# Kernel tuning notes

Measured on AMD Instinct MI355X. Metric: run time of the kernel, lower is better.

The kernel has to match this reference:

```python
import jax, jax.numpy as jnp
import numpy as np

B, C, H, W = 64, 128, 11, 11
OUT = 16
N_SIM = 5
EPS = 1e-2


def _conv3d(x, w, b):
    # x: [b,ci,D,h,w], w: [co,ci,7,3,3], 'same' padding, ReLU
    y = jax.lax.conv_general_dilated(x, w, (1, 1, 1), [(3, 3), (1, 1), (1, 1)],
                                     dimension_numbers=('NCDHW', 'OIDHW', 'NCDHW'))
    return jax.nn.relu(y + b[None, :, None, None, None])


def _conv2d(x, w, b, dil=1):
    p = dil  # 3x3 kernel, 'same' with dilation
    y = jax.lax.conv_general_dilated(x, w, (1, 1), [(p, p), (p, p)], rhs_dilation=(dil, dil),
                                     dimension_numbers=('NCHW', 'OIHW', 'NCHW'))
    return y + b[None, :, None, None]


def _center(f):  # [b,c,h,w] -> [b,c] (center pixel)
    return f[:, :, f.shape[2] // 2, f.shape[3] // 2]


def _ratio(v):  # compute_ratio_withstep: [b,c] -> [b,1,c,c] band-ratio image
    d = v[:, None, :]
    d = jnp.where(jnp.abs(d) < EPS, EPS, d)
    return (v[:, :, None] / d)[:, None, :, :]


def _cpr(sa3d, w):  # CVT3D_2D_SA: spectral-attention collapse [b,16,D,h,w] -> [b,16,h,w]
    a = jax.nn.softmax(w, axis=-1)
    return jax.nn.relu(jnp.einsum('bodhw,od->bohw', sa3d, a))


def _sideout(f2d, w, b):  # sideout2d: mlp on center pixel features
    return _center(f2d) @ w.T + b


def _similar_sum(x, feat, n=N_SIM):
    # topk(n, largest=False) over |feat - center|, gather those pixels from x, sum them
    b, c = x.shape[0], x.shape[1]
    cv = _center(feat).reshape(b, 1, 1, 1)
    diff = jnp.abs(feat - cv).reshape(b, -1)          # [b, h*w]
    _, idx = jax.lax.top_k(-diff, n)                   # n smallest -> [b, n]
    img = x.reshape(b, c, -1)                          # [b, c, h*w]
    idx_b = jnp.broadcast_to(idx[:, None, :], (b, c, n))
    sim = jnp.take_along_axis(img, idx_b, axis=2)      # [b, c, n]
    return sim.sum(axis=2)                             # masked sum over n similar pixels


def _forward(x, w3d1, b3d1, w3d23, b3d23, cpr_w, w2d45, b2d45, seg_w, seg_b,
             so_w, so_b, sp_wa, sp_ba, sp_wb, sp_bb, sp_sw, sp_sb, fuse_para):
    sp_ct = _ratio(_center(x))                         # [b,1,c,c]
    sa1 = _conv3d(x[:, None], w3d1, b3d1)              # [b,16,C,11,11]
    sa1_2d = _cpr(sa1, cpr_w[0])
    sa2 = _conv3d(sa1, w3d23[0], b3d23[0])
    sa2_2d = _cpr(sa2, cpr_w[1])
    sa3 = _conv3d(sa2, w3d23[1], b3d23[1])
    sa3_2d = _cpr(sa3, cpr_w[2])
    sa4_2d = jax.nn.relu(_conv2d(sa3_2d, w2d45[0], b2d45[0]))
    sa5_2d = jax.nn.relu(_conv2d(sa4_2d, w2d45[1], b2d45[1]))

    feats = [sa1_2d, sa2_2d, sa3_2d, sa4_2d, sa5_2d]
    sa_sides, sp_sides = [], []
    for i, f in enumerate(feats):  # fixed 5 structurally-distinct stages
        sa_sides.append(_sideout(f, so_w[i], so_b[i]))
        act = _conv2d(f, seg_w[i], seg_b[i])           # Seg_Conv: [b,1,11,11]
        s = _similar_sum(x, act)                       # [b,C]
        img = jnp.concatenate([_ratio(s), sp_ct], 1)   # [b,2,C,C]
        y = jax.nn.relu(_conv2d(img, sp_wa[i], sp_ba[i], dil=1))
        y = jax.nn.relu(_conv2d(y, sp_wb[i], sp_bb[i], dil=2))
        sp_sides.append(_sideout(y, sp_sw[i], sp_sb[i]))

    sides = sa_sides + sp_sides
    total = sides[0] * fuse_para[0]
    for i in range(1, 10):
        total = total + fuse_para[i] * sides[i]
    return total                                       # [b, OUT]


def setup_inputs() -> dict:
    key = jax.random.key(0)
    ks = jax.random.split(key, 20)
    s = 0.05
    return {
        'x': jax.random.normal(ks[0], (B, C, H, W), jnp.float32),
        'w3d1': jax.random.normal(ks[1], (16, 1, 7, 3, 3), jnp.float32) * s,
        'b3d1': jnp.zeros((16,), jnp.float32),
        'w3d23': jax.random.normal(ks[2], (2, 16, 16, 7, 3, 3), jnp.float32) * s,
        'b3d23': jnp.zeros((2, 16), jnp.float32),
        'cpr_w': jax.random.normal(ks[3], (3, 16, C), jnp.float32) * s,
        'w2d45': jax.random.normal(ks[4], (2, 16, 16, 3, 3), jnp.float32) * s,
        'b2d45': jnp.zeros((2, 16), jnp.float32),
        'seg_w': jax.random.normal(ks[5], (5, 1, 16, 3, 3), jnp.float32) * s,
        'seg_b': jnp.zeros((5, 1), jnp.float32),
        'so_w': jax.random.normal(ks[6], (5, OUT, 16), jnp.float32) * s,
        'so_b': jnp.zeros((5, OUT), jnp.float32),
        'sp_wa': jax.random.normal(ks[7], (5, 16, 2, 3, 3), jnp.float32) * s,
        'sp_ba': jnp.zeros((5, 16), jnp.float32),
        'sp_wb': jax.random.normal(ks[8], (5, 16, 16, 3, 3), jnp.float32) * s,
        'sp_bb': jnp.zeros((5, 16), jnp.float32),
        'sp_sw': jax.random.normal(ks[9], (5, OUT, 16), jnp.float32) * s,
        'sp_sb': jnp.zeros((5, OUT), jnp.float32),
        'fuse_para': jnp.ones((15,), jnp.float32),
    }


def reference(x, w3d1, b3d1, w3d23, b3d23, cpr_w, w2d45, b2d45, seg_w, seg_b,
              so_w, so_b, sp_wa, sp_ba, sp_wb, sp_bb, sp_sw, sp_sb, fuse_para):
    return _forward(x, w3d1, b3d1, w3d23, b3d23, cpr_w, w2d45, b2d45, seg_w, seg_b,
                    so_w, so_b, sp_wa, sp_ba, sp_wb, sp_bb, sp_sw, sp_sb, fuse_para)
```

## Files before the change

### kernel.cpp

```cpp
#include <hip/hip_runtime.h>
#include <hip/hip_bf16.h>


#define F_SLICE (64 * 16 * 121)
#define PKE (64 * 121 * 134 * 16)
#define LHALF 18304
#define AREP_CV 36864

typedef _Float16 half8 __attribute__((ext_vector_type(8)));
typedef float float4v __attribute__((ext_vector_type(4)));
typedef unsigned short u16x8 __attribute__((ext_vector_type(8)));
typedef unsigned short u16x4 __attribute__((ext_vector_type(4)));

typedef __attribute__((address_space(1))) unsigned int gu32;
typedef __attribute__((address_space(3))) unsigned int lu32;

union HU { _Float16 h; unsigned short u; };

__global__ __launch_bounds__(256) void prep_kernel(
    const float* __restrict__ x, const float* __restrict__ cpr_w,
    const float* __restrict__ w3d1, const float* __restrict__ w2d45,
    const float* __restrict__ w3d23, float* __restrict__ x_t,
    float* __restrict__ a_sm, float* __restrict__ wrep1,
    float* __restrict__ wrep2d, unsigned short* __restrict__ arep) {
  const int bx = blockIdx.x, t = threadIdx.x;
  if (bx < 64) {
    __shared__ float tile[128][123];
    const int b = bx;
    const float* xb = x + (size_t)b * 128 * 121;
    for (int idx = t; idx < 128 * 121; idx += 256) {
      int c = idx / 121, p = idx - c * 121;
      tile[c][p] = xb[idx];
    }
    __syncthreads();
    float* ob = x_t + (size_t)b * 121 * 128;
    for (int idx = t; idx < 121 * 128; idx += 256) {
      int p = idx >> 7, c = idx & 127;
      ob[idx] = tile[c][p];
    }
  } else if (bx < 112) {
    __shared__ float red[128];
    const int row = bx - 64;
    float v = (t < 128) ? cpr_w[row * 128 + t] : -3.0e38f;
    if (t < 128) red[t] = v;
    __syncthreads();
    for (int s = 64; s; s >>= 1) {
      if (t < s) red[t] = fmaxf(red[t], red[t + s]);
      __syncthreads();
    }
    float m = red[0];
    __syncthreads();
    float e = (t < 128) ? expf(v - m) : 0.f;
    if (t < 128) red[t] = e;
    __syncthreads();
    for (int s = 64; s; s >>= 1) {
      if (t < s) red[t] += red[t + s];
      __syncthreads();
    }
    if (t < 128) a_sm[row * 128 + t] = e / red[0];
  } else if (bx < 134) {
    int r = (bx - 112) * 256 + t;
    if (r < 1008) {
      int j = r;
      int kw = j % 3; j /= 3;
      int o = j % 8; j /= 8;
      int kh = j % 3; j /= 3;
      int kd = j % 7; j /= 7;
      int gg = j;
      wrep1[r] = w3d1[(gg * 8 + o) * 63 + kd * 9 + kh * 3 + kw];
    } else if (r < 1008 + 4608) {
      int r2 = r - 1008;
      int o = r2 & 15;
      int uv = (r2 >> 4) % 9;
      int ic = (r2 / 144) % 16;
      int layer = r2 / 2304;
      wrep2d[r2] = w2d45[((layer * 16 + o) * 16 + ic) * 9 + uv];
    }
  } else {
    int idx = (bx - 134) * 256 + t;
    if (idx < 2 * AREP_CV) {
      int j = idx & 7;
      int lane = (idx >> 3) & 63;
      int part = (idx >> 9) & 1;
      int rem = idx >> 10;
      int chunk = rem % 36;
      int cv = rem / 36;
      int kw = chunk % 3;
      int grp = chunk / 3;
      int kdp = grp & 3;
      int kh = grp >> 2;
      int m = lane & 15, q = lane >> 4;
      int kd = 2 * kdp + (q >> 1);
      int ic = (q & 1) * 8 + j;
      float w = 0.f;
      if (kd < 7)
        w = w3d23[((cv * 16 + m) * 16 + ic) * 63 + kd * 9 + kh * 3 + kw] *
            256.f;
      _Float16 hi = (_Float16)w;
      HU out;
      out.h = (part == 0) ? hi : (_Float16)(w - (float)hi);
      arep[idx] = out.u;
    }
  }
}

__global__ __launch_bounds__(256, 4) void conv1_kernel(
    const float* __restrict__ in, const float* __restrict__ wrep,
    const float* __restrict__ bias, const float* __restrict__ al,
    unsigned short* __restrict__ pk_hi, unsigned short* __restrict__ pk_lo,
    float* __restrict__ f_out) {
  __shared__ float in_lds[18][134];
  __shared__ float red[2][16][4];
  const int t = threadIdx.x;
  const int bx = blockIdx.x;
  const int b = blockIdx.y;
  const int h = bx / 3;
  const int w0 = (bx % 3) * 4;
  const int lane = t & 63;
  const int wv = t >> 6;
  const int dh = wv & 1;
  const int dd = lane + (dh << 6);
  const int g = __builtin_amdgcn_readfirstlane(wv >> 1);
  const int oc_base = g << 3;

  float acc[8][4];
#pragma unroll
  for (int o = 0; o < 8; ++o)
#pragma unroll
    for (int c = 0; c < 4; ++c) acc[o][c] = 0.f;

  const int ds = t & 127;
  const int half = t >> 7;

  for (int r = half; r < 18; r += 2) {
    int hr = r / 6;
    int wc = r - hr * 6;
    int hh = h - 1 + hr;
    int ww = w0 - 1 + wc;
    bool ok = (hh >= 0) & (hh < 11) & (ww >= 0) & (ww < 11);
    const float* src = in + (((size_t)b) * 121 + hh * 11 + ww) * 128;
    float v = 0.f;
    if (ok && ds >= 3) v = src[ds - 3];
    in_lds[r][ds] = v;
    if (ds < 6) {
      float v2 = 0.f;
      if (ok && ds < 3) v2 = src[125 + ds];
      in_lds[r][128 + ds] = v2;
    }
  }
  __syncthreads();
  const float* wbase = wrep + g * 504;
#pragma unroll
  for (int kd = 0; kd < 7; ++kd) {
#pragma unroll
    for (int kh = 0; kh < 3; ++kh) {
      float ws[24];
      const float* wp = wbase + kd * 72 + kh * 24;
#pragma unroll
      for (int j = 0; j < 24; ++j) ws[j] = wp[j];
      float v[6];
#pragma unroll
      for (int qq = 0; qq < 6; ++qq) v[qq] = in_lds[kh * 6 + qq][dd + kd];
#pragma unroll
      for (int o = 0; o < 8; ++o)
#pragma unroll
        for (int kw = 0; kw < 3; ++kw) {
          float wv_ = ws[o * 3 + kw];
#pragma unroll
          for (int c = 0; c < 4; ++c)
            acc[o][c] = fmaf(wv_, v[kw + c], acc[o][c]);
        }
    }
  }

  const int p0 = h * 11 + w0;
#pragma unroll
  for (int o = 0; o < 8; ++o) {
    float bv = bias[oc_base + o];
#pragma unroll
    for (int c = 0; c < 4; ++c) acc[o][c] = fmaxf(acc[o][c] + bv, 0.f);
  }
#pragma unroll
  for (int c = 0; c < 4; ++c) {
    if (w0 + c < 11) {
      u16x8 hi8, lo8;
#pragma unroll
      for (int o = 0; o < 8; ++o) {
        float s = acc[o][c] * 256.f;
        _Float16 hh = (_Float16)s;
        HU a, bb;
        a.h = hh;
        bb.h = (_Float16)(s - (float)hh);
        hi8[o] = a.u;
        lo8[o] = bb.u;
      }
      size_t base = (((size_t)b * 121 + p0 + c) * 134 + dd + 3) * 16 + oc_base;
      *(u16x8*)&pk_hi[base] = hi8;
      *(u16x8*)&pk_lo[base] = lo8;
    }
  }
  if (dd < 3) {
    u16x8 z = {0, 0, 0, 0, 0, 0, 0, 0};
#pragma unroll
    for (int c = 0; c < 4; ++c) {
      if (w0 + c < 11) {
        size_t b0 = (((size_t)b * 121 + p0 + c) * 134 + dd) * 16 + oc_base;
        size_t b1 =
            (((size_t)b * 121 + p0 + c) * 134 + 131 + dd) * 16 + oc_base;
        *(u16x8*)&pk_hi[b0] = z;
        *(u16x8*)&pk_lo[b0] = z;
        *(u16x8*)&pk_hi[b1] = z;
        *(u16x8*)&pk_lo[b1] = z;
      }
    }
  }
  float alv[8];
#pragma unroll
  for (int o = 0; o < 8; ++o) alv[o] = al[(oc_base + o) * 128 + dd];
#pragma unroll
  for (int o = 0; o < 8; ++o) {
#pragma unroll
    for (int c = 0; c < 4; ++c) {
      float pv = acc[o][c] * alv[o];
#pragma unroll
      for (int off = 32; off; off >>= 1) pv += __shfl_down(pv, off, 64);
      if (lane == 0) red[dh][oc_base + o][c] = pv;
    }
  }
  __syncthreads();
  if (t < 64) {
    int oc = t >> 2, c = t & 3;
    if (w0 + c < 11)
      f_out[((size_t)b * 16 + oc) * 121 + p0 + c] =
          fmaxf(red[0][oc][c] + red[1][oc][c], 0.f);
  }
}

template <bool WRITE_PK>
__global__ __launch_bounds__(512, 2) void conv_mfma_kernel(
    const unsigned short* __restrict__ pin_hi,
    const unsigned short* __restrict__ pin_lo,
    const unsigned short* __restrict__ arep, const float* __restrict__ bias,
    const float* __restrict__ al, unsigned short* __restrict__ pout_hi,
    unsigned short* __restrict__ pout_lo, float* __restrict__ fpart) {
  __shared__ _Float16 lds[2 * LHALF];
  const int t = threadIdx.x;
  const int bx = blockIdx.x, d16 = blockIdx.y, b = blockIdx.z;
  const int lane = t & 63, wave = t >> 6;
  const int n = lane & 15, q = lane >> 4;
  const int hs = wave >> 2, wg = wave & 3;
  const int h = 2 * bx + hs;

#pragma unroll
  for (int i = 0; i < 9; ++i) {
    int u = t + i * 512;
    int lbo = __builtin_amdgcn_readfirstlane((wave << 6) + i * 512);
    if (u < 4576) {
      int part = (u >= 2288) ? 1 : 0;
      int qq = u - part * 2288;
      int pc = qq / 22;
      int dloc = qq - pc * 22;
      int panel = pc >> 1, icq = pc & 1;
      int rr = panel / 13, cc = panel - rr * 13;
      int hh = 2 * bx + rr - 1, ww = cc - 1;
      bool ok = (hh >= 0) & (hh < 11) & (ww >= 0) & (ww < 11);
      if (ok) {
        const unsigned short* srcp = part ? pin_lo : pin_hi;
        const unsigned short* g =
            &srcp[(((size_t)b * 121 + hh * 11 + ww) * 134 + d16 * 16 + dloc) *
                      16 +
                  icq * 8];
        __builtin_amdgcn_global_load_lds((const gu32*)g,
                                         (lu32*)&lds[(size_t)lbo * 8], 16, 0,
                                         0);
      } else {
        u16x8 z = {0, 0, 0, 0, 0, 0, 0, 0};
        *(u16x8*)&lds[(size_t)u * 8] = z;
      }
    }
  }
  float bias_r[4], alr[4];
#pragma unroll
  for (int r = 0; r < 4; ++r) {
    bias_r[r] = bias[q * 4 + r];
    alr[r] = al[(q * 4 + r) * 128 + d16 * 16 + n];
  }
  __syncthreads();

  const int wl0 = wg * 3;
  int cb[5], cbk[5];
  const int base_qn = (q & 1) * 176 + n * 8 + hs * 4576;
  const int kdh = (lane & 32) ? 8 : 0;
#pragma unroll
  for (int j = 0; j < 5; ++j) {
    int colj = wl0 + j;
    if (colj > 12) colj = 12;
    cb[j] = base_qn + colj * 352;
    cbk[j] = cb[j] + kdh;
  }

  float4v acc[3];
#pragma unroll
  for (int tt = 0; tt < 3; ++tt) acc[tt] = (float4v){0.f, 0.f, 0.f, 0.f};

#pragma unroll
  for (int kh = 0; kh < 3; ++kh) {
#pragma unroll
    for (int kdp = 0; kdp < 4; ++kdp) {
      half8 whi[5], wlo[5];
#pragma unroll
      for (int j = 0; j < 5; ++j) {
        int a = ((kdp < 3) ? cbk[j] : cb[j]) + kh * 4576 + kdp * 16;
        whi[j] = *(const half8*)&lds[a];
        wlo[j] = *(const half8*)&lds[a + LHALF];
      }
#pragma unroll
      for (int kw = 0; kw < 3; ++kw) {
        const int c2 = (kh * 4 + kdp) * 3 + kw;
        half8 ahi = *(const half8*)&arep[((c2 * 2 + 0) * 64 + lane) * 8];
        half8 alo = *(const half8*)&arep[((c2 * 2 + 1) * 64 + lane) * 8];
#pragma unroll
        for (int tt = 0; tt < 3; ++tt) {
          const int jj = tt + kw;
          acc[tt] = __builtin_amdgcn_mfma_f32_16x16x32_f16(ahi, whi[jj],
                                                           acc[tt], 0, 0, 0);
          acc[tt] = __builtin_amdgcn_mfma_f32_16x16x32_f16(ahi, wlo[jj],
                                                           acc[tt], 0, 0, 0);
          acc[tt] = __builtin_amdgcn_mfma_f32_16x16x32_f16(alo, whi[jj],
                                                           acc[tt], 0, 0, 0);
        }
      }
    }
  }

#pragma unroll
  for (int tt = 0; tt < 3; ++tt) {
    const int wl = wg * 3 + tt;
    if (h < 11 && wl < 11) {
      const int p = h * 11 + wl;
      float fr[4];
      u16x4 hi4, lo4;
#pragma unroll
      for (int r = 0; r < 4; ++r) {
        float sv = fmaxf(acc[tt][r] * (1.f / 65536.f) + bias_r[r], 0.f);
        fr[r] = sv * alr[r];
        if (WRITE_PK) {
          float s = sv * 256.f;
          _Float16 hh = (_Float16)s;
          HU a, bb;
          a.h = hh;
          bb.h = (_Float16)(s - (float)hh);
          hi4[r] = a.u;
          lo4[r] = bb.u;
        }
      }
      if (WRITE_PK) {
        size_t base =
            (((size_t)b * 121 + p) * 134 + d16 * 16 + n + 3) * 16 + q * 4;
        *(u16x4*)&pout_hi[base] = hi4;
        *(u16x4*)&pout_lo[base] = lo4;
        u16x4 z = {0, 0, 0, 0};
        if (d16 == 0 && n < 3) {
          size_t hb = (((size_t)b * 121 + p) * 134 + n) * 16 + q * 4;
          *(u16x4*)&pout_hi[hb] = z;
          *(u16x4*)&pout_lo[hb] = z;
        }
        if (d16 == 7 && n >= 13) {
          size_t hb = (((size_t)b * 121 + p) * 134 + n + 118) * 16 + q * 4;
          *(u16x4*)&pout_hi[hb] = z;
          *(u16x4*)&pout_lo[hb] = z;
        }
      }
#pragma unroll
      for (int r = 0; r < 4; ++r) {
        float v = fr[r];
        v += __shfl_xor(v, 1, 64);
        v += __shfl_xor(v, 2, 64);
        v += __shfl_xor(v, 4, 64);
        v += __shfl_xor(v, 8, 64);
        if (n == 0)
          fpart[(((size_t)d16 * 64 + b) * 16 + q * 4 + r) * 121 + p] = v;
      }
    }
  }
}

__global__ __launch_bounds__(128) void sp_prep_kernel(
    const float* __restrict__ f1, const float* __restrict__ fpart1,
    const float* __restrict__ fpart2, const float* __restrict__ x_t,
    const float* __restrict__ wrep2d, const float* __restrict__ b2d45,
    const float* __restrict__ seg_w, const float* __restrict__ seg_b,
    const float* __restrict__ so_w, const float* __restrict__ so_b,
    const float* __restrict__ sp_wa, const float* __restrict__ sp_ba,
    const float* __restrict__ sp_wb, const float* __restrict__ sp_bb,
    const float* __restrict__ sp_sw, const float* __restrict__ sp_sb,
    float* __restrict__ sa_sd, float* __restrict__ sp_sd) {
  const int b = blockIdx.x, i = blockIdx.y;
  const int t = threadIdx.x;
  __shared__ float fl[16 * 121];
  __shared__ float buf[16 * 121];
  __shared__ float act[121];
  __shared__ float diffs[121];
  __shared__ int sel[5];
  __shared__ float s7[7], xc7[7];
  __shared__ float P[2][7][7];
  __shared__ float y1[16][9];
  __shared__ float y2[16];

  {
    float* ldst = (i < 3) ? fl : buf;
    if (i == 0) {
      const float* fb = f1 + (size_t)b * 16 * 121;
      for (int idx = t; idx < 16 * 121; idx += 128) ldst[idx] = fb[idx];
    } else {
      const float* fp0 = (i == 1) ? fpart1 : fpart2;
      const size_t boff = (size_t)b * 16 * 121;
      for (int idx = t; idx < 16 * 121; idx += 128) {
        float s = 0.f;
#pragma unroll
        for (int d16 = 0; d16 < 8; ++d16)
          s += fp0[(size_t)d16 * F_SLICE + boff + idx];
        ldst[idx] = fmaxf(s, 0.f);
      }
    }
  }
  __syncthreads();

#define CONV2D_LAYER(SRC, DST, L)                                        \
  if (t < 121) {                                                         \
    int h_ = t / 11, w_ = t - h_ * 11;                                   \
    float a_[16];                                                        \
    _Pragma("unroll") for (int o = 0; o < 16; ++o) a_[o] =               \
        b2d45[(L)*16 + o];                                               \
    for (int ic = 0; ic < 16; ++ic) {                                    \
      _Pragma("unroll") for (int u = 0; u < 3; ++u) {                    \
        int hh_ = h_ + u - 1;                                            \
        _Pragma("unroll") for (int v = 0; v < 3; ++v) {                  \
          int ww_ = w_ + v - 1;                                          \
          float val_ = (hh_ >= 0 && hh_ < 11 && ww_ >= 0 && ww_ < 11)    \
                           ? (SRC)[ic * 121 + hh_ * 11 + ww_]            \
                           : 0.f;                                        \
          const float* wp_ =                                             \
              wrep2d + (((L)*16 + ic) * 9 + u * 3 + v) * 16;             \
          float wr_[16];                                                 \
          _Pragma("unroll") for (int o = 0; o < 16; ++o) wr_[o] = wp_[o];\
          _Pragma("unroll") for (int o = 0; o < 16; ++o) a_[o] =         \
              fmaf(val_, wr_[o], a_[o]);                                 \
        }                                                                \
      }                                                                  \
    }                                                                    \
    _Pragma("unroll") for (int o = 0; o < 16; ++o)(DST)[o * 121 + t] =   \
        fmaxf(a_[o], 0.f);                                               \
  }

  if (i >= 3) {
    CONV2D_LAYER(buf, fl, 0)
    __syncthreads();
    if (i == 4) {
      CONV2D_LAYER(fl, buf, 1)
      __syncthreads();
    }
  }
  const float* F = (i == 4) ? buf : fl;

  if (t < 16) {
    float s = so_b[i * 16 + t];
    const float* swp = so_w + (i * 16 + t) * 16;
    for (int c = 0; c < 16; ++c) s += F[c * 121 + 60] * swp[c];
    sa_sd[((size_t)i * 64 + b) * 16 + t] = s;
  }

  if (t < 121) {
    int h = t / 11, w = t - h * 11;
    float a = seg_b[i];
    const float* sw = seg_w + i * 144;
    for (int ic = 0; ic < 16; ++ic) {
      float w9[9];
#pragma unroll
      for (int j = 0; j < 9; ++j) w9[j] = sw[ic * 9 + j];
#pragma unroll
      for (int u = 0; u < 3; ++u) {
        int hh = h + u - 1;
#pragma unroll
        for (int v = 0; v < 3; ++v) {
          int ww = w + v - 1;
          if (hh >= 0 && hh < 11 && ww >= 0 && ww < 11)
            a = fmaf(F[ic * 121 + hh * 11 + ww], w9[u * 3 + v], a);
        }
      }
    }
    act[t] = a;
  }
  __syncthreads();
  if (t < 121) diffs[t] = fabsf(act[t] - act[60]);
  __syncthreads();

  for (int k = 0; k < 5; ++k) {
    if (t < 64) {
      float d0 = diffs[t];
      int i0 = t;
      float d1 = (t + 64 < 121) ? diffs[t + 64] : 3.0e38f;
      if (d1 < d0) { d0 = d1; i0 = t + 64; }
#pragma unroll
      for (int off = 32; off; off >>= 1) {
        float od = __shfl_down(d0, off, 64);
        int oi = __shfl_down(i0, off, 64);
        if (od < d0 || (od == d0 && oi < i0)) { d0 = od; i0 = oi; }
      }
      if (t == 0) {
        sel[k] = i0;
        diffs[i0] = 3.0e38f;
      }
    }
    __syncthreads();
  }

  if (t < 7) {
    const float* xb = x_t + (size_t)b * 121 * 128;
    float s = 0.f;
    for (int k = 0; k < 5; ++k) s += xb[(size_t)sel[k] * 128 + 61 + t];
    s7[t] = s;
    xc7[t] = xb[60 * 128 + 61 + t];
  }
  __syncthreads();
  if (t < 49) {
    int r = t / 7, c = t - r * 7;
    float d0 = s7[c];
    if (fabsf(d0) < 0.01f) d0 = 0.01f;
    float d1 = xc7[c];
    if (fabsf(d1) < 0.01f) d1 = 0.01f;
    P[0][r][c] = s7[r] / d0;
    P[1][r][c] = xc7[r] / d1;
  }
  __syncthreads();
  for (int item = t; item < 144; item += 128) {
    int ch = item / 9, pos = item - ch * 9;
    int a0 = pos / 3, b0 = pos - a0 * 3;
    float a = sp_ba[i * 16 + ch];
    const float* wa = sp_wa + ((size_t)(i * 16 + ch) * 2) * 9;
#pragma unroll
    for (int icc = 0; icc < 2; ++icc)
#pragma unroll
      for (int u = 0; u < 3; ++u)
#pragma unroll
        for (int v = 0; v < 3; ++v)
          a = fmaf(P[icc][2 * a0 + u][2 * b0 + v], wa[icc * 9 + u * 3 + v], a);
    y1[ch][pos] = fmaxf(a, 0.f);
  }
  __syncthreads();
  if (t < 16) {
    float a = sp_bb[i * 16 + t];
    const float* wb = sp_wb + (size_t)(i * 16 + t) * 16 * 9;
    for (int ch = 0; ch < 16; ++ch)
#pragma unroll
      for (int pos = 0; pos < 9; ++pos)
        a = fmaf(y1[ch][pos], wb[ch * 9 + pos], a);
    y2[t] = fmaxf(a, 0.f);
  }
  __syncthreads();
  if (t < 16) {
    float a = sp_sb[i * 16 + t];
    const float* swp = sp_sw + (size_t)(i * 16 + t) * 16;
    for (int ch = 0; ch < 16; ++ch) a = fmaf(y2[ch], swp[ch], a);
    sp_sd[((size_t)i * 64 + b) * 16 + t] = a;
  }
}

__global__ __launch_bounds__(256) void fuse_kernel(
    const float* __restrict__ sa_sd, const float* __restrict__ sp_sd,
    const float* __restrict__ fp, float* __restrict__ out) {
  int g = blockIdx.x * 256 + threadIdx.x;
  if (g >= 1024) return;
  int b = g >> 4, o = g & 15;
  float tot = 0.f;
  for (int i = 0; i < 5; ++i) {
    tot += fp[i] * sa_sd[((size_t)i * 64 + b) * 16 + o];
    tot += fp[5 + i] * sp_sd[((size_t)i * 64 + b) * 16 + o];
  }
  out[g] = tot;
}

extern "C" void kernel_launch(void* const* d_in, const int* in_sizes, int n_in,
                              void* d_out, int out_size, void* d_ws,
                              size_t ws_size, hipStream_t stream) {
  const float* x = (const float*)d_in[0];
  const float* w3d1 = (const float*)d_in[1];
  const float* b3d1 = (const float*)d_in[2];
  const float* w3d23 = (const float*)d_in[3];
  const float* b3d23 = (const float*)d_in[4];
  const float* cpr_w = (const float*)d_in[5];
  const float* w2d45 = (const float*)d_in[6];
  const float* b2d45 = (const float*)d_in[7];
  const float* seg_w = (const float*)d_in[8];
  const float* seg_b = (const float*)d_in[9];
  const float* so_w = (const float*)d_in[10];
  const float* so_b = (const float*)d_in[11];
  const float* sp_wa = (const float*)d_in[12];
  const float* sp_ba = (const float*)d_in[13];
  const float* sp_wb = (const float*)d_in[14];
  const float* sp_bb = (const float*)d_in[15];
  const float* sp_sw = (const float*)d_in[16];
  const float* sp_sb = (const float*)d_in[17];
  const float* fpar = (const float*)d_in[18];

  float* ws = (float*)d_ws;
  float* x_t = ws;
  float* a_sm = x_t + 991232;
  float* f1 = a_sm + 6144;
  float* fpart1 = f1 + F_SLICE;
  float* fpart2 = fpart1 + 8 * F_SLICE;
  float* sp_sd = fpart2 + 8 * F_SLICE;
  float* sa_sd = sp_sd + 5120;
  float* wrep1 = sa_sd + 5120;
  float* wrep2d = wrep1 + 1024;
  unsigned short* pk1h = (unsigned short*)(wrep2d + 4608);
  unsigned short* pk1l = pk1h + PKE;
  unsigned short* pk2h = pk1l + PKE;
  unsigned short* pk2l = pk2h + PKE;
  unsigned short* arep = pk2l + PKE;

  prep_kernel<<<422, 256, 0, stream>>>(x, cpr_w, w3d1, w2d45, w3d23, x_t,
                                       a_sm, wrep1, wrep2d, arep);

  conv1_kernel<<<dim3(33, 64), 256, 0, stream>>>(x_t, wrep1, b3d1, a_sm, pk1h,
                                                 pk1l, f1);
  conv_mfma_kernel<true><<<dim3(6, 8, 64), 512, 0, stream>>>(
      pk1h, pk1l, arep, b3d23, a_sm + 2048, pk2h, pk2l, fpart1);
  conv_mfma_kernel<false><<<dim3(6, 8, 64), 512, 0, stream>>>(
      pk2h, pk2l, arep + AREP_CV, b3d23 + 16, a_sm + 4096, nullptr, nullptr,
      fpart2);

  sp_prep_kernel<<<dim3(64, 5), 128, 0, stream>>>(
      f1, fpart1, fpart2, x_t, wrep2d, b2d45, seg_w, seg_b, so_w, so_b,
      sp_wa, sp_ba, sp_wb, sp_bb, sp_sw, sp_sb, sa_sd, sp_sd);
  fuse_kernel<<<4, 256, 0, stream>>>(sa_sd, sp_sd, fpar, (float*)d_out);
}
```

Measured before the change: 448.8 us.

## Move first 3D conv onto MFMA with split-fp16 inputs and padded layout

The first 3D convolution (1 input channel, 16 outputs) is rewritten from scalar FMA on fp32 into MFMA 16x16x32 f16 ops. The prep kernel now also emits a depth-padded hi/lo fp16 copy of x and packed hi/lo weights with the kd taps on the K dimension. The conv1 output is written as per-depth-chunk partial sums like the later layers, and sp_prep sums them. The hi/lo split keeps accuracy close to fp32 at the cost of three MFMAs per tile, extra workspace traffic for the padded input, and reuse of the fpart1 buffer as scratch.

```diff
diff --git a/kernel.cpp b/kernel.cpp
--- a/kernel.cpp
+++ b/kernel.cpp
@@ -6,6 +6,7 @@
 #define PKE (64 * 121 * 134 * 16)
 #define LHALF 18304
 #define AREP_CV 36864
+#define XPADE (64 * 121 * 136)
 
 typedef _Float16 half8 __attribute__((ext_vector_type(8)));
 typedef float float4v __attribute__((ext_vector_type(4)));
@@ -21,8 +22,9 @@
     const float* __restrict__ x, const float* __restrict__ cpr_w,
     const float* __restrict__ w3d1, const float* __restrict__ w2d45,
     const float* __restrict__ w3d23, float* __restrict__ x_t,
-    float* __restrict__ a_sm, float* __restrict__ wrep1,
-    float* __restrict__ wrep2d, unsigned short* __restrict__ arep) {
+    float* __restrict__ a_sm, float* __restrict__ wrep2d,
+    unsigned short* __restrict__ arep, unsigned short* __restrict__ arep1,
+    unsigned short* __restrict__ xpadh, unsigned short* __restrict__ xpadl) {
   const int bx = blockIdx.x, t = threadIdx.x;
   if (bx < 64) {
     __shared__ float tile[128][123];
@@ -37,6 +39,19 @@
     for (int idx = t; idx < 121 * 128; idx += 256) {
       int p = idx >> 7, c = idx & 127;
       ob[idx] = tile[c][p];
+    }
+    unsigned short* xh = xpadh + (size_t)b * 16456;
+    unsigned short* xl = xpadl + (size_t)b * 16456;
+    for (int idx = t; idx < 16456; idx += 256) {
+      int p = idx / 136, d = idx - p * 136;
+      float v = 0.f;
+      if (d >= 3 && d < 131) v = tile[d - 3][p] * 256.f;
+      _Float16 hi = (_Float16)v;
+      HU a2, b2;
+      a2.h = hi;
+      b2.h = (_Float16)(v - (float)hi);
+      xh[idx] = a2.u;
+      xl[idx] = b2.u;
     }
   } else if (bx < 112) {
     __shared__ float red[128];
@@ -58,18 +73,22 @@
       __syncthreads();
     }
     if (t < 128) a_sm[row * 128 + t] = e / red[0];
-  } else if (bx < 134) {
+  } else if (bx < 142) {
     int r = (bx - 112) * 256 + t;
-    if (r < 1008) {
-      int j = r;
-      int kw = j % 3; j /= 3;
-      int o = j % 8; j /= 8;
-      int kh = j % 3; j /= 3;
-      int kd = j % 7; j /= 7;
-      int gg = j;
-      wrep1[r] = w3d1[(gg * 8 + o) * 63 + kd * 9 + kh * 3 + kw];
-    } else if (r < 1008 + 4608) {
-      int r2 = r - 1008;
+    if (r < 3072) {
+      int j = r & 7;
+      int lane = (r >> 3) & 63;
+      int part = (r >> 9) & 1;
+      int kh = r >> 10;
+      int m = lane & 15, q = lane >> 4;
+      float w = 0.f;
+      if (q < 3 && j < 7) w = w3d1[m * 63 + j * 9 + kh * 3 + q] * 256.f;
+      _Float16 hi = (_Float16)w;
+      HU o;
+      o.h = part ? (_Float16)(w - (float)hi) : hi;
+      arep1[r] = o.u;
+    } else if (r < 3072 + 4608) {
+      int r2 = r - 3072;
       int o = r2 & 15;
       int uv = (r2 >> 4) % 9;
       int ic = (r2 / 144) % 16;
@@ -77,7 +96,7 @@
       wrep2d[r2] = w2d45[((layer * 16 + o) * 16 + ic) * 9 + uv];
     }
   } else {
-    int idx = (bx - 134) * 256 + t;
+    int idx = (bx - 142) * 256 + t;
     if (idx < 2 * AREP_CV) {
       int j = idx & 7;
       int lane = (idx >> 3) & 63;
@@ -104,135 +123,155 @@
   }
 }
 
-__global__ __launch_bounds__(256, 4) void conv1_kernel(
-    const float* __restrict__ in, const float* __restrict__ wrep,
-    const float* __restrict__ bias, const float* __restrict__ al,
-    unsigned short* __restrict__ pk_hi, unsigned short* __restrict__ pk_lo,
-    float* __restrict__ f_out) {
-  __shared__ float in_lds[18][134];
-  __shared__ float red[2][16][4];
+__global__ __launch_bounds__(512, 2) void conv1_mfma_kernel(
+    const unsigned short* __restrict__ xph,
+    const unsigned short* __restrict__ xpl,
+    const unsigned short* __restrict__ arep1, const float* __restrict__ bias,
+    const float* __restrict__ al, unsigned short* __restrict__ pk_hi,
+    unsigned short* __restrict__ pk_lo, float* __restrict__ fpart) {
+  __shared__ _Float16 lds1[104 * 256];
   const int t = threadIdx.x;
-  const int bx = blockIdx.x;
-  const int b = blockIdx.y;
-  const int h = bx / 3;
-  const int w0 = (bx % 3) * 4;
-  const int lane = t & 63;
-  const int wv = t >> 6;
-  const int dh = wv & 1;
-  const int dd = lane + (dh << 6);
-  const int g = __builtin_amdgcn_readfirstlane(wv >> 1);
-  const int oc_base = g << 3;
-
-  float acc[8][4];
-#pragma unroll
-  for (int o = 0; o < 8; ++o)
-#pragma unroll
-    for (int c = 0; c < 4; ++c) acc[o][c] = 0.f;
-
-  const int ds = t & 127;
-  const int half = t >> 7;
-
-  for (int r = half; r < 18; r += 2) {
-    int hr = r / 6;
-    int wc = r - hr * 6;
-    int hh = h - 1 + hr;
-    int ww = w0 - 1 + wc;
-    bool ok = (hh >= 0) & (hh < 11) & (ww >= 0) & (ww < 11);
-    const float* src = in + (((size_t)b) * 121 + hh * 11 + ww) * 128;
-    float v = 0.f;
-    if (ok && ds >= 3) v = src[ds - 3];
-    in_lds[r][ds] = v;
-    if (ds < 6) {
-      float v2 = 0.f;
-      if (ok && ds < 3) v2 = src[125 + ds];
-      in_lds[r][128 + ds] = v2;
-    }
-  }
-  __syncthreads();
-  const float* wbase = wrep + g * 504;
-#pragma unroll
-  for (int kd = 0; kd < 7; ++kd) {
+  const int bx = blockIdx.x, gy = blockIdx.y, b = blockIdx.z;
+  const int lane = t & 63, wave = t >> 6;
+  const int n = lane & 15, q = lane >> 4;
+  const int hs = wave >> 2, wg = wave & 3;
+  const int h = 2 * bx + hs;
+  const int D0 = gy * 32;
+
+  {
+    const int g = t & 31;
+    const int s = g & 7;
+    const int w0 = t >> 5;
+#pragma unroll
+    for (int k = 0; k < 7; ++k) {
+      int wid = w0 + k * 16;
+      if (wid < 104) {
+        int part = wid >= 52;
+        int w2 = wid - part * 52;
+        int rr = w2 / 13;
+        int cc = w2 - rr * 13;
+        int hh = 2 * bx - 1 + rr, ww = cc - 1;
+        u16x8 v0 = {0, 0, 0, 0, 0, 0, 0, 0};
+        u16x8 v1 = {0, 0, 0, 0, 0, 0, 0, 0};
+        if (hh >= 0 && hh < 11 && ww >= 0 && ww < 11) {
+          const unsigned short* src = (part ? xpl : xph) +
+                                      ((size_t)b * 121 + hh * 11 + ww) * 136 +
+                                      D0 + (g & ~7);
+          v0 = *(const u16x8*)src;
+          v1 = *(const u16x8*)(src + 8);
+        }
+        u16x8 ov;
+#define SHIFT_CASE(S)                                                   \
+  case S: {                                                             \
+    _Pragma("unroll") for (int e = 0; e < 8; ++e) ov[e] =               \
+        (((S) + e) < 8) ? v0[((S) + e) & 7] : v1[((S) + e) & 7];        \
+  } break;
+        switch (s) {
+          SHIFT_CASE(0)
+          SHIFT_CASE(1)
+          SHIFT_CASE(2)
+          SHIFT_CASE(3)
+          SHIFT_CASE(4)
+          SHIFT_CASE(5)
+          SHIFT_CASE(6)
+          SHIFT_CASE(7)
+        }
+#undef SHIFT_CASE
+        *(u16x8*)&lds1[wid * 256 + g * 8] = ov;
+      }
+    }
+  }
+
+  half8 ahi[3], alo[3];
+#pragma unroll
+  for (int kh = 0; kh < 3; ++kh) {
+    ahi[kh] = *(const half8*)&arep1[(kh * 2 + 0) * 512 + lane * 8];
+    alo[kh] = *(const half8*)&arep1[(kh * 2 + 1) * 512 + lane * 8];
+  }
+  int colq[3];
+#pragma unroll
+  for (int tt = 0; tt < 3; ++tt) {
+    int c = wg * 3 + tt + q;
+    colq[tt] = (c > 12) ? 12 : c;
+  }
+  float bias_r[4];
+#pragma unroll
+  for (int r = 0; r < 4; ++r) bias_r[r] = bias[q * 4 + r];
+  __syncthreads();
+
+#pragma unroll
+  for (int d16loc = 0; d16loc < 2; ++d16loc) {
+    const int d16g = gy * 2 + d16loc;
+    const int dbase = d16loc * 16 + n;
+    float4v acc[3];
+#pragma unroll
+    for (int tt = 0; tt < 3; ++tt) acc[tt] = (float4v){0.f, 0.f, 0.f, 0.f};
 #pragma unroll
     for (int kh = 0; kh < 3; ++kh) {
-      float ws[24];
-      const float* wp = wbase + kd * 72 + kh * 24;
-#pragma unroll
-      for (int j = 0; j < 24; ++j) ws[j] = wp[j];
-      float v[6];
-#pragma unroll
-      for (int qq = 0; qq < 6; ++qq) v[qq] = in_lds[kh * 6 + qq][dd + kd];
-#pragma unroll
-      for (int o = 0; o < 8; ++o)
-#pragma unroll
-        for (int kw = 0; kw < 3; ++kw) {
-          float wv_ = ws[o * 3 + kw];
-#pragma unroll
-          for (int c = 0; c < 4; ++c)
-            acc[o][c] = fmaf(wv_, v[kw + c], acc[o][c]);
-        }
-    }
-  }
-
-  const int p0 = h * 11 + w0;
-#pragma unroll
-  for (int o = 0; o < 8; ++o) {
-    float bv = bias[oc_base + o];
-#pragma unroll
-    for (int c = 0; c < 4; ++c) acc[o][c] = fmaxf(acc[o][c] + bv, 0.f);
-  }
-#pragma unroll
-  for (int c = 0; c < 4; ++c) {
-    if (w0 + c < 11) {
-      u16x8 hi8, lo8;
-#pragma unroll
-      for (int o = 0; o < 8; ++o) {
-        float s = acc[o][c] * 256.f;
-        _Float16 hh = (_Float16)s;
-        HU a, bb;
-        a.h = hh;
-        bb.h = (_Float16)(s - (float)hh);
-        hi8[o] = a.u;
-        lo8[o] = bb.u;
-      }
-      size_t base = (((size_t)b * 121 + p0 + c) * 134 + dd + 3) * 16 + oc_base;
-      *(u16x8*)&pk_hi[base] = hi8;
-      *(u16x8*)&pk_lo[base] = lo8;
-    }
-  }
-  if (dd < 3) {
-    u16x8 z = {0, 0, 0, 0, 0, 0, 0, 0};
-#pragma unroll
-    for (int c = 0; c < 4; ++c) {
-      if (w0 + c < 11) {
-        size_t b0 = (((size_t)b * 121 + p0 + c) * 134 + dd) * 16 + oc_base;
-        size_t b1 =
-            (((size_t)b * 121 + p0 + c) * 134 + 131 + dd) * 16 + oc_base;
-        *(u16x8*)&pk_hi[b0] = z;
-        *(u16x8*)&pk_lo[b0] = z;
-        *(u16x8*)&pk_hi[b1] = z;
-        *(u16x8*)&pk_lo[b1] = z;
-      }
-    }
-  }
-  float alv[8];
-#pragma unroll
-  for (int o = 0; o < 8; ++o) alv[o] = al[(oc_base + o) * 128 + dd];
-#pragma unroll
-  for (int o = 0; o < 8; ++o) {
-#pragma unroll
-    for (int c = 0; c < 4; ++c) {
-      float pv = acc[o][c] * alv[o];
-#pragma unroll
-      for (int off = 32; off; off >>= 1) pv += __shfl_down(pv, off, 64);
-      if (lane == 0) red[dh][oc_base + o][c] = pv;
-    }
-  }
-  __syncthreads();
-  if (t < 64) {
-    int oc = t >> 2, c = t & 3;
-    if (w0 + c < 11)
-      f_out[((size_t)b * 16 + oc) * 121 + p0 + c] =
-          fmaxf(red[0][oc][c] + red[1][oc][c], 0.f);
+      const int rowoff = (hs + kh) * 13;
+#pragma unroll
+      for (int tt = 0; tt < 3; ++tt) {
+        const int wid = rowoff + colq[tt];
+        half8 bh = *(const half8*)&lds1[wid * 256 + dbase * 8];
+        half8 bl = *(const half8*)&lds1[(wid + 52) * 256 + dbase * 8];
+        acc[tt] =
+            __builtin_amdgcn_mfma_f32_16x16x32_f16(ahi[kh], bh, acc[tt], 0, 0, 0);
+        acc[tt] =
+            __builtin_amdgcn_mfma_f32_16x16x32_f16(ahi[kh], bl, acc[tt], 0, 0, 0);
+        acc[tt] =
+            __builtin_amdgcn_mfma_f32_16x16x32_f16(alo[kh], bh, acc[tt], 0, 0, 0);
+      }
+    }
+    float alr[4];
+#pragma unroll
+    for (int r = 0; r < 4; ++r)
+      alr[r] = al[(q * 4 + r) * 128 + d16g * 16 + n];
+#pragma unroll
+    for (int tt = 0; tt < 3; ++tt) {
+      const int wl = wg * 3 + tt;
+      if (h < 11 && wl < 11) {
+        const int p = h * 11 + wl;
+        float fr[4];
+        u16x4 hi4, lo4;
+#pragma unroll
+        for (int r = 0; r < 4; ++r) {
+          float sv = fmaxf(acc[tt][r] * (1.f / 65536.f) + bias_r[r], 0.f);
+          fr[r] = sv * alr[r];
+          float sc = sv * 256.f;
+          _Float16 hh = (_Float16)sc;
+          HU a2, b2;
+          a2.h = hh;
+          b2.h = (_Float16)(sc - (float)hh);
+          hi4[r] = a2.u;
+          lo4[r] = b2.u;
+        }
+        size_t base =
+            (((size_t)b * 121 + p) * 134 + d16g * 16 + n + 3) * 16 + q * 4;
+        *(u16x4*)&pk_hi[base] = hi4;
+        *(u16x4*)&pk_lo[base] = lo4;
+        u16x4 z = {0, 0, 0, 0};
+        if (d16g == 0 && n < 3) {
+          size_t hb = (((size_t)b * 121 + p) * 134 + n) * 16 + q * 4;
+          *(u16x4*)&pk_hi[hb] = z;
+          *(u16x4*)&pk_lo[hb] = z;
+        }
+        if (d16g == 7 && n >= 13) {
+          size_t hb = (((size_t)b * 121 + p) * 134 + n + 118) * 16 + q * 4;
+          *(u16x4*)&pk_hi[hb] = z;
+          *(u16x4*)&pk_lo[hb] = z;
+        }
+#pragma unroll
+        for (int r = 0; r < 4; ++r) {
+          float v = fr[r];
+          v += __shfl_xor(v, 1, 64);
+          v += __shfl_xor(v, 2, 64);
+          v += __shfl_xor(v, 4, 64);
+          v += __shfl_xor(v, 8, 64);
+          if (n == 0)
+            fpart[(((size_t)d16g * 64 + b) * 16 + q * 4 + r) * 121 + p] = v;
+        }
+      }
+    }
   }
 }
 
@@ -386,7 +425,7 @@
 }
 
 __global__ __launch_bounds__(128) void sp_prep_kernel(
-    const float* __restrict__ f1, const float* __restrict__ fpart1,
+    const float* __restrict__ fpart0, const float* __restrict__ fpart1,
     const float* __restrict__ fpart2, const float* __restrict__ x_t,
     const float* __restrict__ wrep2d, const float* __restrict__ b2d45,
     const float* __restrict__ seg_w, const float* __restrict__ seg_b,
@@ -409,19 +448,14 @@
 
   {
     float* ldst = (i < 3) ? fl : buf;
-    if (i == 0) {
-      const float* fb = f1 + (size_t)b * 16 * 121;
-      for (int idx = t; idx < 16 * 121; idx += 128) ldst[idx] = fb[idx];
-    } else {
-      const float* fp0 = (i == 1) ? fpart1 : fpart2;
-      const size_t boff = (size_t)b * 16 * 121;
-      for (int idx = t; idx < 16 * 121; idx += 128) {
-        float s = 0.f;
-#pragma unroll
-        for (int d16 = 0; d16 < 8; ++d16)
-          s += fp0[(size_t)d16 * F_SLICE + boff + idx];
-        ldst[idx] = fmaxf(s, 0.f);
-      }
+    const float* fp0 = (i == 0) ? fpart0 : (i == 1) ? fpart1 : fpart2;
+    const size_t boff = (size_t)b * 16 * 121;
+    for (int idx = t; idx < 16 * 121; idx += 128) {
+      float s = 0.f;
+#pragma unroll
+      for (int d16 = 0; d16 < 8; ++d16)
+        s += fp0[(size_t)d16 * F_SLICE + boff + idx];
+      ldst[idx] = fmaxf(s, 0.f);
     }
   }
   __syncthreads();
@@ -606,24 +640,27 @@
   float* ws = (float*)d_ws;
   float* x_t = ws;
   float* a_sm = x_t + 991232;
-  float* f1 = a_sm + 6144;
-  float* fpart1 = f1 + F_SLICE;
+  float* fpart0 = a_sm + 6144;
+  float* fpart1 = fpart0 + 8 * F_SLICE;
   float* fpart2 = fpart1 + 8 * F_SLICE;
   float* sp_sd = fpart2 + 8 * F_SLICE;
   float* sa_sd = sp_sd + 5120;
-  float* wrep1 = sa_sd + 5120;
-  float* wrep2d = wrep1 + 1024;
+  float* wrep2d = sa_sd + 5120;
   unsigned short* pk1h = (unsigned short*)(wrep2d + 4608);
   unsigned short* pk1l = pk1h + PKE;
   unsigned short* pk2h = pk1l + PKE;
   unsigned short* pk2l = pk2h + PKE;
   unsigned short* arep = pk2l + PKE;
-
-  prep_kernel<<<422, 256, 0, stream>>>(x, cpr_w, w3d1, w2d45, w3d23, x_t,
-                                       a_sm, wrep1, wrep2d, arep);
-
-  conv1_kernel<<<dim3(33, 64), 256, 0, stream>>>(x_t, wrep1, b3d1, a_sm, pk1h,
-                                                 pk1l, f1);
+  unsigned short* arep1 = arep + 2 * AREP_CV;
+  unsigned short* xpadh = (unsigned short*)fpart1;
+  unsigned short* xpadl = xpadh + XPADE;
+
+  prep_kernel<<<430, 256, 0, stream>>>(x, cpr_w, w3d1, w2d45, w3d23, x_t,
+                                       a_sm, wrep2d, arep, arep1, xpadh,
+                                       xpadl);
+
+  conv1_mfma_kernel<<<dim3(6, 4, 64), 512, 0, stream>>>(
+      xpadh, xpadl, arep1, b3d1, a_sm, pk1h, pk1l, fpart0);
   conv_mfma_kernel<true><<<dim3(6, 8, 64), 512, 0, stream>>>(
       pk1h, pk1l, arep, b3d23, a_sm + 2048, pk2h, pk2l, fpart1);
   conv_mfma_kernel<false><<<dim3(6, 8, 64), 512, 0, stream>>>(
@@ -631,7 +668,7 @@
       fpart2);
 
   sp_prep_kernel<<<dim3(64, 5), 128, 0, stream>>>(
-      f1, fpart1, fpart2, x_t, wrep2d, b2d45, seg_w, seg_b, so_w, so_b,
+      fpart0, fpart1, fpart2, x_t, wrep2d, b2d45, seg_w, seg_b, so_w, so_b,
       sp_wa, sp_ba, sp_wb, sp_bb, sp_sw, sp_sb, sa_sd, sp_sd);
   fuse_kernel<<<4, 256, 0, stream>>>(sa_sd, sp_sd, fpar, (float*)d_out);
 }
```

Result: faster. 422.0 us (-6.0%).
